# Performance work log

Hardware: AMD Instinct MI355X
Metric: run time of the kernel (lower is better)

Reference implementation:

```python
import jax, jax.numpy as jnp
import numpy as np

N1 = 8000   # solute nodes
N2 = 8000   # solvent nodes
E = 128000  # edges per graph side (avg degree 16)
B = 128     # number of graphs in the batch
NFEAT, NHID, NCLS = 128, 256, 512
D = 2 * NCLS   # Set2Set input dim (1024)
H = D          # LSTM hidden = input_dim in DGL Set2Set


def setup_inputs() -> dict:
    key = jax.random.key(0)
    ks = jax.random.split(key, 24)
    w = lambda k, shp, fan: (jax.random.normal(k, shp, jnp.float32) / np.sqrt(fan))
    inp = {}
    inp["x1"] = jax.random.normal(ks[0], (N1, NFEAT), jnp.float32)
    inp["x2"] = jax.random.normal(ks[1], (N2, NFEAT), jnp.float32)
    inp["src1"] = jax.random.randint(ks[2], (E,), 0, N1, jnp.int32)
    inp["dst1"] = jax.random.randint(ks[3], (E,), 0, N1, jnp.int32)
    inp["src2"] = jax.random.randint(ks[4], (E,), 0, N2, jnp.int32)
    inp["dst2"] = jax.random.randint(ks[5], (E,), 0, N2, jnp.int32)
    inp["gid1"] = jnp.sort(jax.random.randint(ks[6], (N1,), 0, B, jnp.int32))
    inp["gid2"] = jnp.sort(jax.random.randint(ks[7], (N2,), 0, B, jnp.int32))
    # GraphConv weights (DGL stores W as [in, out]) + biases
    inp["W_gc1"] = w(ks[8], (NFEAT, NHID), NFEAT); inp["b_gc1"] = jnp.zeros((NHID,), jnp.float32)
    inp["W_gc2"] = w(ks[9], (NHID, NCLS), NHID);   inp["b_gc2"] = jnp.zeros((NCLS,), jnp.float32)
    inp["W_gc3"] = w(ks[10], (NFEAT, NHID), NFEAT); inp["b_gc3"] = jnp.zeros((NHID,), jnp.float32)
    inp["W_gc4"] = w(ks[11], (NHID, NCLS), NHID);   inp["b_gc4"] = jnp.zeros((NCLS,), jnp.float32)
    # Set2Set LSTM (input = 2*D, hidden = H), torch gate order i,f,g,o
    inp["W_ih"] = w(ks[12], (4 * H, 2 * D), 2 * D)
    inp["W_hh"] = w(ks[13], (4 * H, H), H)
    inp["b_ih"] = jnp.zeros((4 * H,), jnp.float32)
    inp["b_hh"] = jnp.zeros((4 * H,), jnp.float32)
    # MLP head
    inp["W_fc1"] = w(ks[14], (1024, 4096), 4096); inp["b_fc1"] = jnp.zeros((1024,), jnp.float32)
    inp["W_fc2"] = w(ks[15], (512, 1024), 1024);  inp["b_fc2"] = jnp.zeros((512,), jnp.float32)
    inp["W_fc3"] = w(ks[16], (1, 512), 512);      inp["b_fc3"] = jnp.zeros((1,), jnp.float32)
    return inp


def _gconv(x, src, dst, W, b, n):
    # DGL GraphConv, norm='both': D_out^{-1/2} scaling at src, sum over in-edges, D_in^{-1/2} at dst
    ones = jnp.ones(src.shape[0], x.dtype)
    outd = jnp.clip(jax.ops.segment_sum(ones, src, num_segments=n), 1.0)
    ind = jnp.clip(jax.ops.segment_sum(ones, dst, num_segments=n), 1.0)
    h = (x * (outd ** -0.5)[:, None]) @ W
    agg = jax.ops.segment_sum(h[src], dst, num_segments=n)   # sparse neighbor aggregation
    return agg * (ind ** -0.5)[:, None] + b


def _set2set(x, gid, Wih, Whh, bih, bhh):
    # DGL Set2Set, n_iters=2, 1-layer LSTM; x: [N, D], gid: [N] graph membership
    d = x.shape[1]
    q_star = jnp.zeros((B, 2 * d), x.dtype)
    h = jnp.zeros((B, d), x.dtype)
    c = jnp.zeros((B, d), x.dtype)
    for _ in range(2):
        gates = q_star @ Wih.T + h @ Whh.T + bih + bhh
        i, f, g, o = jnp.split(gates, 4, axis=1)
        c = jax.nn.sigmoid(f) * c + jax.nn.sigmoid(i) * jnp.tanh(g)
        h = jax.nn.sigmoid(o) * jnp.tanh(c)
        e = jnp.sum(x * h[gid], axis=1)                       # per-node attention logit
        m = jax.ops.segment_max(e, gid, num_segments=B)
        ex = jnp.exp(e - m[gid])
        s = jax.ops.segment_sum(ex, gid, num_segments=B)
        alpha = ex / s[gid]                                   # segment softmax
        r = jax.ops.segment_sum(alpha[:, None] * x, gid, num_segments=B)
        q_star = jnp.concatenate([h, r], axis=1)
    return q_star


def reference(x1, x2, src1, dst1, src2, dst2, gid1, gid2,
              W_gc1, b_gc1, W_gc2, b_gc2, W_gc3, b_gc3, W_gc4, b_gc4,
              W_ih, W_hh, b_ih, b_hh,
              W_fc1, b_fc1, W_fc2, b_fc2, W_fc3, b_fc3):
    s = jax.nn.relu(_gconv(x1, src1, dst1, W_gc1, b_gc1, N1))
    s = _gconv(s, src1, dst1, W_gc2, b_gc2, N1)
    v = jax.nn.relu(_gconv(x2, src2, dst2, W_gc3, b_gc3, N2))
    v = _gconv(v, src2, dst2, W_gc4, b_gc4, N2)
    # len_map = len1.T @ len2 == same-graph indicator for binary membership matrices
    len_map = (gid1[:, None] == gid2[None, :]).astype(s.dtype)
    imap = jnp.tanh(s @ v.T) * len_map                        # [N1, N2]
    solvent_prime = imap.T @ s                                # [N2, NCLS]
    solute_prime = imap @ v                                   # [N1, NCLS]
    sf = jnp.concatenate([s, solute_prime], axis=1)           # [N1, 2*NCLS]
    vf = jnp.concatenate([v, solvent_prime], axis=1)
    ss = _set2set(sf, gid1, W_ih, W_hh, b_ih, b_hh)           # [B, 4*NCLS]
    vs = _set2set(vf, gid2, W_ih, W_hh, b_ih, b_hh)
    z = jnp.concatenate([ss, vs], axis=1)                     # [B, 4096]
    z = jax.nn.relu(z @ W_fc1.T + b_fc1)
    z = jax.nn.relu(z @ W_fc2.T + b_fc2)
    return z @ W_fc3.T + b_fc3                                # [B, 1]
```

## Files before the change

kernel.cpp:

```cpp
#include <hip/hip_runtime.h>

#define DEV __device__ __forceinline__

typedef _Float16 half8 __attribute__((ext_vector_type(8)));
typedef _Float16 half4_t __attribute__((ext_vector_type(4)));
typedef float f32x4 __attribute__((ext_vector_type(4)));

DEV float ftanh(float x){
  float ax = fabsf(x);
  float e = __expf(-2.f*ax);
  float t = (1.f - e)/(1.f + e);
  return x < 0.f ? -t : t;
}
DEV float fsigm(float x){ return 1.f/(1.f + expf(-x)); }
DEV float wredsum(float v){
  #pragma unroll
  for (int o=32;o;o>>=1) v += __shfl_xor(v,o,64);
  return v;
}
DEV f32x4 MF(half8 a, half8 b, f32x4 c){
  return __builtin_amdgcn_mfma_f32_16x16x32_f16(a,b,c,0,0,0);
}
DEV void split8(float4 a0, float4 a1, half8& h, half8& l){
  float f[8] = {a0.x,a0.y,a0.z,a0.w,a1.x,a1.y,a1.z,a1.w};
  #pragma unroll
  for (int e=0;e<8;++e){
    _Float16 hh = (_Float16)f[e];
    h[e] = hh;
    l[e] = (_Float16)(f[e] - (float)hh);
  }
}

__global__ void k_zero_i32(int* __restrict__ p, int n){
  int i = blockIdx.x*256 + threadIdx.x; if (i<n) p[i]=0;
}

__global__ void k_hist2(const int* __restrict__ s1, const int* __restrict__ d1, int E1,
                        int* __restrict__ co1, int* __restrict__ ci1,
                        const int* __restrict__ s2, const int* __restrict__ d2, int E2,
                        int* __restrict__ co2, int* __restrict__ ci2){
  int e = blockIdx.x*256 + threadIdx.x;
  if (e < E1){ atomicAdd(&co1[s1[e]],1); atomicAdd(&ci1[d1[e]],1); }
  int f = e - E1;
  if (f >= 0 && f < E2){ atomicAdd(&co2[s2[f]],1); atomicAdd(&ci2[d2[f]],1); }
}

__global__ void k_scan2(const int* __restrict__ c1, int n1, int* __restrict__ r1,
                        const int* __restrict__ c2, int n2, int* __restrict__ r2){
  __shared__ int sm[1024];
  const int* cnt = blockIdx.x ? c2 : c1;
  int*       row = blockIdx.x ? r2 : r1;
  int n          = blockIdx.x ? n2 : n1;
  int t = threadIdx.x;
  int per = n/1024 + 1;
  int st = t*per;
  int s = 0;
  for (int i=st;i<st+per;++i) if (i<n) s += cnt[i];
  sm[t]=s; __syncthreads();
  for (int o=1;o<1024;o<<=1){
    int v = (t>=o)? sm[t-o]:0;
    __syncthreads();
    sm[t] += v;
    __syncthreads();
  }
  int base = sm[t]-s;
  for (int i=st;i<st+per;++i){
    if (i<=n) row[i]=base;
    if (i<n) base += cnt[i];
  }
}

__global__ void k_scale2(const int* __restrict__ co1, const int* __restrict__ ci1, int n1,
                         float* __restrict__ os1, float* __restrict__ is1,
                         const int* __restrict__ co2, const int* __restrict__ ci2, int n2,
                         float* __restrict__ os2, float* __restrict__ is2){
  int i = blockIdx.x*256+threadIdx.x;
  if (i<n1){
    int a = co1[i] > 1 ? co1[i] : 1;
    int b = ci1[i] > 1 ? ci1[i] : 1;
    os1[i] = 1.f/sqrtf((float)a);
    is1[i] = 1.f/sqrtf((float)b);
  }
  int j = i - n1;
  if (j>=0 && j<n2){
    int a = co2[j] > 1 ? co2[j] : 1;
    int b = ci2[j] > 1 ? ci2[j] : 1;
    os2[j] = 1.f/sqrtf((float)a);
    is2[j] = 1.f/sqrtf((float)b);
  }
}

__global__ void k_scatter2(const int* __restrict__ s1, const int* __restrict__ d1, int E1,
                           const int* __restrict__ row1, int* __restrict__ cur1, int* __restrict__ csr1,
                           const int* __restrict__ s2, const int* __restrict__ d2, int E2,
                           const int* __restrict__ row2, int* __restrict__ cur2, int* __restrict__ csr2){
  int e = blockIdx.x*256+threadIdx.x;
  if (e<E1){ int d=d1[e]; int p=atomicAdd(&cur1[d],1); csr1[row1[d]+p]=s1[e]; }
  int f = e - E1;
  if (f>=0 && f<E2){ int d=d2[f]; int p=atomicAdd(&cur2[d],1); csr2[row2[d]+p]=s2[f]; }
}

__global__ void k_goff2(const int* __restrict__ g1, int n1, int* __restrict__ o1,
                        const int* __restrict__ g2, int n2, int* __restrict__ o2, int B,
                        int* __restrict__ pb1, int* __restrict__ gm1,
                        int* __restrict__ pb2, int* __restrict__ gm2){
  __shared__ int sc[2][256];
  int t = threadIdx.x;
  const int* gid = (t>=256)? g2 : g1;
  int*      goff = (t>=256)? o2 : o1;
  int n          = (t>=256)? n2 : n1;
  const int side = t>>8, q = t & 255;
  if (q<=B){
    int lo=0, hi=n;
    while (lo<hi){ int mid=(lo+hi)>>1; if (gid[mid]<q) lo=mid+1; else hi=mid; }
    goff[q]=lo;
  }
  __syncthreads();
  int pc = 0;
  if (q < B){
    const int* go = side ? o2 : o1;
    int c = go[q+1]-go[q]; if (c>128) c=128;
    pc = (c+31)&~31;
  }
  sc[side][q] = pc;
  __syncthreads();
  for (int o=1;o<B;o<<=1){
    int v = (q>=o && q<B) ? sc[side][q-o] : 0;
    __syncthreads();
    if (q<B) sc[side][q] += v;
    __syncthreads();
  }
  if (q < B){
    int incl = sc[side][q];
    int pbv  = incl - pc;
    int* pb = side ? pb2 : pb1;
    int* gm = side ? gm2 : gm1;
    pb[q] = pbv;
    if (q == B-1) pb[B] = incl;
    int nb = pc>>5, b0 = pbv>>5;
    for (int k=0;k<nb;++k) gm[b0+k] = q;
  }
}

__global__ void k_agg_h(const float* __restrict__ x, int ldx, const float* __restrict__ osc,
                        const int* __restrict__ row, const int* __restrict__ csr,
                        _Float16* __restrict__ oh, _Float16* __restrict__ ol, int n, int f4shift){
  int F4 = 1<<f4shift;
  int node = blockIdx.x*(256>>f4shift) + (threadIdx.x>>f4shift);
  if (node>=n) return;
  int fc = threadIdx.x & (F4-1);
  int F = F4<<2;
  int rs=row[node], re=row[node+1];
  float ax=0, ay=0, az=0, aw=0;
  if (osc){
    for (int e=rs;e<re;++e){
      int s = csr[e];
      float sc = osc[s];
      const float4 v = *(const float4*)(x + (size_t)s*ldx + (fc<<2));
      ax += sc*v.x; ay += sc*v.y; az += sc*v.z; aw += sc*v.w;
    }
  } else {
    int e = rs;
    for (; e+1<re; e+=2){
      int s0 = csr[e], s1 = csr[e+1];
      const float4 v0 = *(const float4*)(x + (size_t)s0*ldx + (fc<<2));
      const float4 v1 = *(const float4*)(x + (size_t)s1*ldx + (fc<<2));
      ax += v0.x+v1.x; ay += v0.y+v1.y; az += v0.z+v1.z; aw += v0.w+v1.w;
    }
    if (e<re){
      int s0 = csr[e];
      const float4 v0 = *(const float4*)(x + (size_t)s0*ldx + (fc<<2));
      ax += v0.x; ay += v0.y; az += v0.z; aw += v0.w;
    }
  }
  half4_t hv, lv;
  hv.x = (_Float16)ax; lv.x = (_Float16)(ax - (float)hv.x);
  hv.y = (_Float16)ay; lv.y = (_Float16)(ay - (float)hv.y);
  hv.z = (_Float16)az; lv.z = (_Float16)(az - (float)hv.z);
  hv.w = (_Float16)aw; lv.w = (_Float16)(aw - (float)hv.w);
  size_t o = (size_t)node*F + (fc<<2);
  *(half4_t*)(oh + o) = hv;
  *(half4_t*)(ol + o) = lv;
}

__global__ void k_wpack4(const float* __restrict__ W0, const float* __restrict__ W1,
                         const float* __restrict__ W2, const float* __restrict__ W3,
                         _Float16* __restrict__ h0, _Float16* __restrict__ l0,
                         _Float16* __restrict__ h1, _Float16* __restrict__ l1,
                         _Float16* __restrict__ h2, _Float16* __restrict__ l2,
                         _Float16* __restrict__ h3, _Float16* __restrict__ l3){
  int w = blockIdx.y;
  const float* W = (w==0)?W0:(w==1)?W1:(w==2)?W2:W3;
  _Float16* oh = (w==0)?h0:(w==1)?h1:(w==2)?h2:h3;
  _Float16* ol = (w==0)?l0:(w==1)?l1:(w==2)?l2:l3;
  int K   = (w&1)? 256 : 128;
  int nsh = (w&1)? 9 : 8;
  int i = blockIdx.x*256 + threadIdx.x;
  if (i >= (K<<nsh)) return;
  int k = i >> nsh, n = i & ((1<<nsh)-1);
  float v = W[i];
  _Float16 h = (_Float16)v;
  _Float16 l = (_Float16)(v - (float)h);
  size_t p = (((size_t)(k>>3)<<nsh) + n)*8 + (k&7);
  oh[p] = h; ol[p] = l;
}

__global__ __launch_bounds__(256)
void k_wpackT(const float* __restrict__ W, int ldw, int N,
              _Float16* __restrict__ Bh, _Float16* __restrict__ Bl){
  __shared__ float st[32][260];
  const int k0 = (int)blockIdx.x << 8;
  const int n0 = (int)blockIdx.y << 5;
  const int t = threadIdx.x;
  const int r = t >> 3, la = t & 7;
  const float* src = W + (size_t)(n0 + r)*ldw + k0;
  #pragma unroll
  for (int q=0;q<8;++q){
    int f = (la<<2) + (q<<5);
    *(float4*)&st[r][f] = *(const float4*)(src + f);
  }
  __syncthreads();
  const int nl = t & 31;
  #pragma unroll
  for (int j=0;j<4;++j){
    int kbl = (t>>5) + (j<<3);
    half8 h8, l8;
    #pragma unroll
    for (int e=0;e<8;++e){
      float v = st[nl][(kbl<<3)+e];
      _Float16 hh = (_Float16)v;
      h8[e]=hh; l8[e]=(_Float16)(v-(float)hh);
    }
    size_t a = ((size_t)((k0>>3)+kbl)*N + n0 + nl)*8;
    *(half8*)(Bh + a) = h8;
    *(half8*)(Bl + a) = l8;
  }
}

__global__ __launch_bounds__(256)
void k_gconv_mfma(const _Float16* __restrict__ Ah0, const _Float16* __restrict__ Al0,
                  const _Float16* __restrict__ Ah1, const _Float16* __restrict__ Al1,
                  const _Float16* __restrict__ Bh0, const _Float16* __restrict__ Bl0,
                  const _Float16* __restrict__ Bh1, const _Float16* __restrict__ Bl1,
                  float* __restrict__ C0, float* __restrict__ C1, int ldc,
                  int M0, int M1, int N, int K,
                  const float* __restrict__ rs0, const float* __restrict__ rs1,
                  const float* __restrict__ bi0, const float* __restrict__ bi1, int relu,
                  const float* __restrict__ po0, const float* __restrict__ po1)
{
  __shared__ __align__(16) _Float16 As[2][4096];
  __shared__ __align__(16) _Float16 Bs[2][4096];

  const int gx = gridDim.x, gxy = gridDim.x*gridDim.y;
  const int nwg = gxy*2;
  int fid = blockIdx.x + gx*blockIdx.y + gxy*blockIdx.z;
  int q = nwg>>3, r = nwg&7;
  int xcd = fid & 7, idx = fid >> 3;
  int sid = (xcd<r ? xcd*(q+1) : r*(q+1)+(xcd-r)*q) + idx;
  const int z  = sid / gxy;  int rem = sid - z*gxy;
  const int by = rem / gx,  bx = rem - by*gx;

  const _Float16* Ah = z ? Ah1 : Ah0;
  const _Float16* Al = z ? Al1 : Al0;
  const _Float16* Bh = z ? Bh1 : Bh0;
  const _Float16* Bl = z ? Bl1 : Bl0;
  float*       C  = z ? C1 : C0;
  const float* rsc = z ? rs1 : rs0;
  const float* bia = z ? bi1 : bi0;
  const float* po  = z ? po1 : po0;
  const int M = z ? M1 : M0;

  const int row0 = by << 7;
  const int col0 = bx << 7;
  if (row0 >= ((M+127)&~127)) return;

  const int tid = threadIdx.x;
  const int am  = tid >> 2;
  const int akb = tid & 3;
  const int bn  = tid & 127;
  const int bkb = tid >> 7;
  const int wid = tid >> 6, lane = tid & 63;
  const int wr = wid >> 1, wc = wid & 1;
  const int lr = lane & 15, lg = lane >> 4;

  const size_t ldb8 = (size_t)N * 8;
  f32x4 acc[4][4] = {};

  const int kpt = K >> 5;
  const int nt  = 3 * kpt;

  half8 ga0, ga1, gb0, gb1;
  {
    const _Float16* Ap = Ah + (size_t)(row0 + am) * K + (akb<<3);
    ga0 = *(const half8*)(Ap);
    ga1 = *(const half8*)(Ap + (size_t)64 * K);
    const _Float16* Bp = Bh + (size_t)bkb * ldb8 + (size_t)(col0 + bn) * 8;
    gb0 = *(const half8*)(Bp);
    gb1 = *(const half8*)(Bp + 2*ldb8);
  }
  *(half8*)&As[0][(akb*128 + am)*8]        = ga0;
  *(half8*)&As[0][(akb*128 + am + 64)*8]   = ga1;
  *(half8*)&Bs[0][(bkb*128 + bn)*8]        = gb0;
  *(half8*)&Bs[0][((bkb+2)*128 + bn)*8]    = gb1;
  __syncthreads();

  int term = 0, kk = 32;
  if (kk == K){ kk = 0; term = 1; }
  for (int t = 0; t < nt; ++t){
    const int cb = t & 1;
    if (t + 1 < nt){
      const _Float16* Asrc = (term == 1) ? Al : Ah;
      const _Float16* Bsrc = (term == 2) ? Bl : Bh;
      const _Float16* Ap = Asrc + (size_t)(row0 + am) * K + kk + (akb<<3);
      ga0 = *(const half8*)(Ap);
      ga1 = *(const half8*)(Ap + (size_t)64 * K);
      const _Float16* Bp = Bsrc + (size_t)((kk>>3) + bkb) * ldb8 + (size_t)(col0 + bn) * 8;
      gb0 = *(const half8*)(Bp);
      gb1 = *(const half8*)(Bp + 2*ldb8);
      kk += 32; if (kk == K){ kk = 0; ++term; }
    }
    {
      const _Float16* Abase = &As[cb][((lg<<7) + (wr<<6) + lr)<<3];
      const _Float16* Bbase = &Bs[cb][((lg<<7) + (wc<<6) + lr)<<3];
      half8 af[4], bf[4];
      #pragma unroll
      for (int i=0;i<4;++i){
        af[i] = *(const half8*)(Abase + i*128);
        bf[i] = *(const half8*)(Bbase + i*128);
      }
      #pragma unroll
      for (int mi=0; mi<4; ++mi){
        #pragma unroll
        for (int ni=0; ni<4; ++ni){
          acc[mi][ni] = __builtin_amdgcn_mfma_f32_16x16x32_f16(af[mi], bf[ni], acc[mi][ni], 0, 0, 0);
        }
      }
    }
    if (t + 1 < nt){
      const int nb_ = cb ^ 1;
      *(half8*)&As[nb_][(akb*128 + am)*8]      = ga0;
      *(half8*)&As[nb_][(akb*128 + am + 64)*8] = ga1;
      *(half8*)&Bs[nb_][(bkb*128 + bn)*8]      = gb0;
      *(half8*)&Bs[nb_][((bkb+2)*128 + bn)*8]  = gb1;
    }
    __syncthreads();
  }

  #pragma unroll
  for (int ni = 0; ni < 4; ++ni){
    int cc = col0 + (wc<<6) + (ni<<4) + lr;
    float bv = bia ? bia[cc] : 0.f;
    #pragma unroll
    for (int mi = 0; mi < 4; ++mi){
      int rbase = row0 + (wr<<6) + (mi<<4) + (lg<<2);
      #pragma unroll
      for (int j = 0; j < 4; ++j){
        int rr = rbase + j;
        if (rr < M){
          float rs_ = rsc ? rsc[rr] : 1.f;
          float v = acc[mi][ni][j]*rs_ + bv;
          if (relu) v = fmaxf(v, 0.f);
          if (po) v *= po[rr];
          C[(size_t)rr*ldc + cc] = v;
        }
      }
    }
  }
}

__global__ __launch_bounds__(256)
void k_pack(const float* __restrict__ sf, const float* __restrict__ vf,
            const int* __restrict__ go1, const int* __restrict__ go2,
            const int* __restrict__ pb1, const int* __restrict__ pb2,
            const int* __restrict__ gm1, const int* __restrict__ gm2,
            _Float16* __restrict__ p1h, _Float16* __restrict__ p1l,
            _Float16* __restrict__ p2h, _Float16* __restrict__ p2l, int B)
{
  __shared__ float st[32][516];
  const int side = blockIdx.y;
  const float* x = side ? vf : sf;
  const int* go = side ? go2 : go1;
  const int* pb = side ? pb2 : pb1;
  const int* gm = side ? gm2 : gm1;
  _Float16* ph = side ? p2h : p1h;
  _Float16* pl = side ? p2l : p1l;
  const int u = blockIdx.x;
  if (u*32 >= pb[B]) return;
  const int g = gm[u];
  const int j0 = u*32 - pb[g];
  const int base = go[g];
  int cnt = go[g+1]-base; if (cnt>128) cnt=128;
  const int t = threadIdx.x;
  const int r = t>>3, f0 = (t&7)<<2;
  const bool valid = (j0 + r) < cnt;
  const float* src = x + (size_t)(base + j0 + r)*1024;
  #pragma unroll
  for (int q=0;q<16;++q){
    int f = f0 + (q<<5);
    float4 vv;
    if (valid) vv = *(const float4*)(src + f);
    else { vv.x=0.f; vv.y=0.f; vv.z=0.f; vv.w=0.f; }
    *(float4*)&st[r][f] = vv;
  }
  __syncthreads();
  #pragma unroll
  for (int q=0;q<8;++q){
    int u2 = t + (q<<8);
    int jg = u2>>9, f = u2&511;
    half8 h8, l8;
    #pragma unroll
    for (int e=0;e<8;++e){
      float vvv = st[(jg<<3)+e][f];
      _Float16 hh = (_Float16)vvv;
      h8[e]=hh; l8[e]=(_Float16)(vvv-(float)hh);
    }
    size_t a = ((size_t)((u<<2)+jg)<<12) + ((size_t)f<<3);
    *(half8*)(ph + a) = h8;
    *(half8*)(pl + a) = l8;
  }
}

__global__ __launch_bounds__(256)
void k_T(const float* __restrict__ sf, const float* __restrict__ vf,
         const int* __restrict__ go1, const int* __restrict__ go2,
         _Float16* __restrict__ Th, _Float16* __restrict__ Tl, int B)
{
  __shared__ __align__(16) _Float16 Ahs[64*136 + 8];
  __shared__ __align__(16) _Float16 Als[64*136 + 8];
  __shared__ __align__(16) _Float16 Bhs[2][2048];
  __shared__ __align__(16) _Float16 Bls[2][2048];
  const int g = blockIdx.x, rt = blockIdx.y;
  int gR = go1[g]; int c1 = go1[g+1]-gR; if (c1>128) c1=128;
  int gO = go2[g]; int c2 = go2[g+1]-gO; if (c2>128) c2=128;
  const int c1_32 = (c1+31)&~31, c2_32 = (c2+31)&~31;
  if ((rt<<4) >= c1_32 || c2_32 == 0) return;
  const int tid = threadIdx.x;
  {
    const int r = tid >> 4;
    const int f0 = (tid & 15) << 5;
    const int row = (rt<<4) + r;
    const bool val = row < c1;
    const float* src = sf + (size_t)(gR + row)*1024 + f0;
    #pragma unroll
    for (int q=0;q<4;++q){
      float4 v0, v1;
      if (val){
        v0 = *(const float4*)(src + (q<<3));
        v1 = *(const float4*)(src + (q<<3) + 4);
      } else {
        v0.x=0.f; v0.y=0.f; v0.z=0.f; v0.w=0.f; v1 = v0;
      }
      half8 h,l; split8(v0,v1,h,l);
      const int a = ((f0>>3) + q)*136 + (r<<3);
      *(half8*)&Ahs[a] = h; *(half8*)&Als[a] = l;
    }
  }
  const int w = tid>>6, lane = tid&63, lr = lane&15, lg = lane>>4;
  const int bc = tid>>2, bfg = tid&3, bf = bfg<<3;
  const int bwr = (bfg<<9) + ((bc ^ (bfg<<2))<<3);
  const int ncc = (c2_32 + 63) >> 6;
  _Float16* T0h = Th + ((size_t)g<<14);
  _Float16* T0l = Tl + ((size_t)g<<14);
  _Float16* T1h = Th + ((size_t)(B + g)<<14);
  _Float16* T1l = Tl + ((size_t)(B + g)<<14);
  for (int cc=0; cc<ncc; ++cc){
    const int cbase = cc<<6;
    const int colr = cbase + bc;
    const bool bval = colr < c2;
    const float* bsrc = vf + (size_t)(gO + colr)*1024 + bf;
    {
      float4 v0, v1;
      if (bval){ v0 = *(const float4*)(bsrc); v1 = *(const float4*)(bsrc + 4); }
      else { v0.x=0.f; v0.y=0.f; v0.z=0.f; v0.w=0.f; v1 = v0; }
      half8 h,l; split8(v0,v1,h,l);
      *(half8*)&Bhs[0][bwr] = h; *(half8*)&Bls[0][bwr] = l;
    }
    __syncthreads();
    f32x4 acc = {0.f,0.f,0.f,0.f};
    const int col_l = (w<<4) + lr;
    const int ba = (lg<<9) + ((col_l ^ (lg<<2))<<3);
    for (int kc=0; kc<16; ++kc){
      float4 p0, p1;
      if (kc+1<16){
        if (bval){
          const float* s = bsrc + ((kc+1)<<5);
          p0 = *(const float4*)s; p1 = *(const float4*)(s + 4);
        } else { p0.x=0.f; p0.y=0.f; p0.z=0.f; p0.w=0.f; p1 = p0; }
      }
      const int aa = ((kc<<2)+lg)*136 + (lr<<3);
      half8 ah = *(const half8*)&Ahs[aa];
      half8 al = *(const half8*)&Als[aa];
      half8 bh = *(const half8*)&Bhs[kc&1][ba];
      half8 bl = *(const half8*)&Bls[kc&1][ba];
      acc = MF(ah,bh,acc);
      acc = MF(al,bh,acc);
      acc = MF(ah,bl,acc);
      if (kc+1<16){
        half8 h,l; split8(p0,p1,h,l);
        *(half8*)&Bhs[(kc+1)&1][bwr] = h; *(half8*)&Bls[(kc+1)&1][bwr] = l;
      }
      __syncthreads();
    }
    const int col = cbase + col_l;
    if (col < c2_32){
      half4_t t1h, t1l;
      #pragma unroll
      for (int qq=0;qq<4;++qq){
        int r = (rt<<4) + (lg<<2) + qq;
        float t = (r < c1 && col < c2) ? ftanh(acc[qq]) : 0.f;
        _Float16 hh = (_Float16)t;
        _Float16 ll = (_Float16)(t - (float)hh);
        T0h[(r<<7) + col] = hh;
        T0l[(r<<7) + col] = ll;
        t1h[qq] = hh; t1l[qq] = ll;
      }
      const int r0 = (rt<<4) + (lg<<2);
      *(half4_t*)&T1h[(col<<7) + r0] = t1h;
      *(half4_t*)&T1l[(col<<7) + r0] = t1l;
    }
  }
}

__global__ __launch_bounds__(256)
void k_apply(const _Float16* __restrict__ Th, const _Float16* __restrict__ Tl,
             const _Float16* __restrict__ p1h, const _Float16* __restrict__ p1l,
             const _Float16* __restrict__ p2h, const _Float16* __restrict__ p2l,
             const int* __restrict__ go1, const int* __restrict__ go2,
             const int* __restrict__ pb1, const int* __restrict__ pb2,
             float* __restrict__ sf, float* __restrict__ vf, int B)
{
  const int side = blockIdx.x, g = blockIdx.y, ft = blockIdx.z;
  const int* goR = side ? go2 : go1;
  const int* goO = side ? go1 : go2;
  const int* pbO = side ? pb1 : pb2;
  const _Float16* oph = side ? p1h : p2h;
  const _Float16* opl = side ? p1l : p2l;
  float* outp = side ? vf : sf;
  int gR = goR[g]; int cR = goR[g+1]-gR; if (cR>128) cR=128;
  int gO = goO[g]; int cO = goO[g+1]-gO; if (cO>128) cO=128;
  if (cR <= 0) return;
  const int pO = pbO[g];
  const int cO32 = (cO+31)&~31;
  const int MR = ((cR+15)&~15)>>4;
  const _Float16* Tph = Th + ((size_t)(side*B + g)<<14);
  const _Float16* Tpl = Tl + ((size_t)(side*B + g)<<14);
  const int tid = threadIdx.x, w = tid>>6, lane = tid&63;
  const int lr = lane&15, lg = lane>>4;
  const int f0 = (ft<<8) + (w<<6);
  for (int rc = 0; rc < MR; rc += 4){
    f32x4 acc[4][4];
    #pragma unroll
    for (int a_=0;a_<4;++a_)
      #pragma unroll
      for (int b_=0;b_<4;++b_) acc[a_][b_] = (f32x4){0.f,0.f,0.f,0.f};
    for (int k0=0; k0<cO32; k0+=32){
      half8 bh[4], bl[4];
      #pragma unroll
      for (int nj=0;nj<4;++nj){
        size_t a = ((size_t)((pO + k0)>>3) + lg)*4096 + (size_t)(f0 + (nj<<4) + lr)*8;
        bh[nj] = *(const half8*)(oph + a);
        bl[nj] = *(const half8*)(opl + a);
      }
      #pragma unroll
      for (int mi=0;mi<4;++mi){
        if (rc + mi < MR){
          int a = ((((rc+mi)<<4) + lr)<<7) + k0 + (lg<<3);
          half8 th_ = *(const half8*)&Tph[a];
          half8 tl_ = *(const half8*)&Tpl[a];
          #pragma unroll
          for (int nj=0;nj<4;++nj){
            acc[mi][nj] = MF(th_, bh[nj], acc[mi][nj]);
            acc[mi][nj] = MF(tl_, bh[nj], acc[mi][nj]);
            acc[mi][nj] = MF(th_, bl[nj], acc[mi][nj]);
          }
        }
      }
    }
    #pragma unroll
    for (int mi=0;mi<4;++mi){
      if (rc + mi < MR){
        #pragma unroll
        for (int nj=0;nj<4;++nj){
          #pragma unroll
          for (int qq=0;qq<4;++qq){
            int r = (((rc+mi)<<4)) + (lg<<2) + qq;
            if (r < cR)
              outp[(size_t)(gR + r)*1024 + 512 + f0 + (nj<<4) + lr] = acc[mi][nj][qq];
          }
        }
      }
    }
  }
}

__global__ __launch_bounds__(256)
void k_gemmsk(const float* __restrict__ Ab, size_t AsideOff, int lda,
              const float* __restrict__ Bm, int ldb,
              float* __restrict__ P, int M, int N, int kchunk)
{
  __shared__ float As[2][16][132];
  __shared__ float Bs[2][16][68];
  const int tid = threadIdx.x;
  const int col0 = (int)blockIdx.x << 6;
  const int kbeg = (int)blockIdx.z * kchunk;
  const float* A = Ab + (size_t)blockIdx.y * AsideOff;
  const int ar = tid >> 1, ak = (tid & 1) << 3;
  const int br = tid >> 2, bk = (tid & 3) << 2;
  const int tx = tid & 15, ty = tid >> 4;
  const float* Arow = A + (size_t)ar * lda + kbeg + ak;
  const float* Brow = Bm + (size_t)(col0 + br) * ldb + kbeg + bk;
  float acc[8][4] = {};
  float4 a0 = *(const float4*)(Arow);
  float4 a1 = *(const float4*)(Arow + 4);
  float4 b0 = *(const float4*)(Brow);
  As[0][ak+0][ar]=a0.x; As[0][ak+1][ar]=a0.y; As[0][ak+2][ar]=a0.z; As[0][ak+3][ar]=a0.w;
  As[0][ak+4][ar]=a1.x; As[0][ak+5][ar]=a1.y; As[0][ak+6][ar]=a1.z; As[0][ak+7][ar]=a1.w;
  Bs[0][bk+0][br]=b0.x; Bs[0][bk+1][br]=b0.y; Bs[0][bk+2][br]=b0.z; Bs[0][bk+3][br]=b0.w;
  __syncthreads();
  const int nt = kchunk >> 4;
  for (int t = 0; t < nt; ++t){
    const int cb = t & 1;
    if (t + 1 < nt){
      int k0 = (t + 1) << 4;
      a0 = *(const float4*)(Arow + k0);
      a1 = *(const float4*)(Arow + k0 + 4);
      b0 = *(const float4*)(Brow + k0);
    }
    #pragma unroll
    for (int kk = 0; kk < 16; ++kk){
      float4 b4 = *(const float4*)&Bs[cb][kk][tx << 2];
      float4 a4 = *(const float4*)&As[cb][kk][ty << 3];
      float4 a5 = *(const float4*)&As[cb][kk][(ty << 3) + 4];
      acc[0][0]+=a4.x*b4.x; acc[0][1]+=a4.x*b4.y; acc[0][2]+=a4.x*b4.z; acc[0][3]+=a4.x*b4.w;
      acc[1][0]+=a4.y*b4.x; acc[1][1]+=a4.y*b4.y; acc[1][2]+=a4.y*b4.z; acc[1][3]+=a4.y*b4.w;
      acc[2][0]+=a4.z*b4.x; acc[2][1]+=a4.z*b4.y; acc[2][2]+=a4.z*b4.z; acc[2][3]+=a4.z*b4.w;
      acc[3][0]+=a4.w*b4.x; acc[3][1]+=a4.w*b4.y; acc[3][2]+=a4.w*b4.z; acc[3][3]+=a4.w*b4.w;
      acc[4][0]+=a5.x*b4.x; acc[4][1]+=a5.x*b4.y; acc[4][2]+=a5.x*b4.z; acc[4][3]+=a5.x*b4.w;
      acc[5][0]+=a5.y*b4.x; acc[5][1]+=a5.y*b4.y; acc[5][2]+=a5.y*b4.z; acc[5][3]+=a5.y*b4.w;
      acc[6][0]+=a5.z*b4.x; acc[6][1]+=a5.z*b4.y; acc[6][2]+=a5.z*b4.z; acc[6][3]+=a5.z*b4.w;
      acc[7][0]+=a5.w*b4.x; acc[7][1]+=a5.w*b4.y; acc[7][2]+=a5.w*b4.z; acc[7][3]+=a5.w*b4.w;
    }
    if (t + 1 < nt){
      const int nb = cb ^ 1;
      As[nb][ak+0][ar]=a0.x; As[nb][ak+1][ar]=a0.y; As[nb][ak+2][ar]=a0.z; As[nb][ak+3][ar]=a0.w;
      As[nb][ak+4][ar]=a1.x; As[nb][ak+5][ar]=a1.y; As[nb][ak+6][ar]=a1.z; As[nb][ak+7][ar]=a1.w;
      Bs[nb][bk+0][br]=b0.x; Bs[nb][bk+1][br]=b0.y; Bs[nb][bk+2][br]=b0.z; Bs[nb][bk+3][br]=b0.w;
    }
    __syncthreads();
  }
  float* Pz = P + (size_t)(blockIdx.y*gridDim.z + blockIdx.z) * M * N;
  #pragma unroll
  for (int i = 0; i < 8; ++i){
    int rr = (ty << 3) + i;
    float4 v = {acc[i][0], acc[i][1], acc[i][2], acc[i][3]};
    *(float4*)(Pz + (size_t)rr*N + col0 + (tx<<2)) = v;
  }
}

__global__ __launch_bounds__(256)
void k_gemmsk_h(const float* __restrict__ Ab, size_t AsideOff, int lda,
                const _Float16* __restrict__ Bhp, const _Float16* __restrict__ Blp,
                float* __restrict__ P, int N, int kchunk)
{
  __shared__ __align__(16) _Float16 Ahs[2][4096];
  __shared__ __align__(16) _Float16 Als[2][4096];
  const int tid = threadIdx.x;
  const int col0 = (int)blockIdx.x << 7;
  const int kbeg = (int)blockIdx.z * kchunk;
  const float* A = Ab + (size_t)blockIdx.y * AsideOff;
  const int ar = tid >> 1, aq = (tid & 1) << 4;
  const int wid = tid>>6, lane = tid&63;
  const int wr = wid>>1, wc = wid&1;
  const int lr = lane&15, lg = lane>>4;
  const float* Arow = A + (size_t)ar*lda + kbeg + aq;
  const int akb = aq>>3;
  f32x4 acc[4][4] = {};
  const int nc = kchunk >> 5;
  float4 g0,g1,g2,g3;
  g0 = *(const float4*)(Arow);     g1 = *(const float4*)(Arow+4);
  g2 = *(const float4*)(Arow+8);   g3 = *(const float4*)(Arow+12);
  {
    half8 h,l;
    split8(g0,g1,h,l);
    *(half8*)&Ahs[0][(akb*128+ar)*8] = h;     *(half8*)&Als[0][(akb*128+ar)*8] = l;
    split8(g2,g3,h,l);
    *(half8*)&Ahs[0][((akb+1)*128+ar)*8] = h; *(half8*)&Als[0][((akb+1)*128+ar)*8] = l;
  }
  __syncthreads();
  for (int c=0;c<nc;++c){
    const int cb = c&1;
    if (c+1<nc){
      const float* p = Arow + ((c+1)<<5);
      g0 = *(const float4*)(p);    g1 = *(const float4*)(p+4);
      g2 = *(const float4*)(p+8);  g3 = *(const float4*)(p+12);
    }
    const size_t kb0 = (size_t)((kbeg + (c<<5)) >> 3) + lg;
    half8 bh[4], bl[4];
    #pragma unroll
    for (int ni=0;ni<4;++ni){
      size_t a = (kb0*N + col0 + (wc<<6) + (ni<<4) + lr)*8;
      bh[ni] = *(const half8*)(Bhp + a);
      bl[ni] = *(const half8*)(Blp + a);
    }
    #pragma unroll
    for (int mi=0;mi<4;++mi){
      int aa = ((lg<<7) + (wr<<6) + (mi<<4) + lr)<<3;
      half8 ah = *(const half8*)&Ahs[cb][aa];
      half8 al = *(const half8*)&Als[cb][aa];
      #pragma unroll
      for (int ni=0;ni<4;++ni){
        acc[mi][ni] = MF(ah,bh[ni],acc[mi][ni]);
        acc[mi][ni] = MF(al,bh[ni],acc[mi][ni]);
        acc[mi][ni] = MF(ah,bl[ni],acc[mi][ni]);
      }
    }
    if (c+1<nc){
      const int nb = cb^1;
      half8 h,l;
      split8(g0,g1,h,l);
      *(half8*)&Ahs[nb][(akb*128+ar)*8] = h;     *(half8*)&Als[nb][(akb*128+ar)*8] = l;
      split8(g2,g3,h,l);
      *(half8*)&Ahs[nb][((akb+1)*128+ar)*8] = h; *(half8*)&Als[nb][((akb+1)*128+ar)*8] = l;
    }
    __syncthreads();
  }
  float* Pz = P + (size_t)(blockIdx.y*gridDim.z + blockIdx.z)*128*N;
  #pragma unroll
  for (int mi=0;mi<4;++mi){
    #pragma unroll
    for (int ni=0;ni<4;++ni){
      int cc2 = col0 + (wc<<6) + (ni<<4) + lr;
      #pragma unroll
      for (int j=0;j<4;++j){
        int rr2 = (wr<<6) + (mi<<4) + (lg<<2) + j;
        Pz[(size_t)rr2*N + cc2] = acc[mi][ni][j];
      }
    }
  }
}

__global__ void k_red_bias(const float* __restrict__ P, int split, int MN, int N,
                           const float* __restrict__ bias, float* __restrict__ C, int relu){
  int i = blockIdx.x*256 + threadIdx.x;
  if (i >= MN) return;
  float v = bias[i & (N-1)];
  for (int s=0;s<split;++s) v += P[(size_t)s*MN + i];
  if (relu) v = fmaxf(v, 0.f);
  C[i] = v;
}

__global__ void k_lstm1(const float* __restrict__ bih, const float* __restrict__ bhh,
                        float* __restrict__ c1, float* __restrict__ h1){
  int j = blockIdx.x*256 + threadIdx.x;
  if (j >= 1024) return;
  float gi = bih[j]        + bhh[j];
  float gg = bih[j+2048]   + bhh[j+2048];
  float go = bih[j+3072]   + bhh[j+3072];
  float cc = fsigm(gi)*ftanh(gg);
  c1[j] = cc;
  h1[j] = fsigm(go)*ftanh(cc);
}

__global__ void k_gemv_u(const float* __restrict__ Wih, const float* __restrict__ Whh,
                         const float* __restrict__ bih, const float* __restrict__ bhh,
                         const float* __restrict__ h1, float* __restrict__ u){
  int w = (blockIdx.x*256 + threadIdx.x)>>6;
  int lane = threadIdx.x & 63;
  if (w >= 4096) return;
  const float* wi = Wih + (size_t)w*2048;
  const float* wh = Whh + (size_t)w*1024;
  float acc = 0.f;
  #pragma unroll
  for (int qq=0;qq<4;++qq){
    int o = qq*256 + (lane<<2);
    float4 hv = *(const float4*)(h1 + o);
    float4 a  = *(const float4*)(wi + o);
    float4 b  = *(const float4*)(wh + o);
    acc += hv.x*(a.x+b.x) + hv.y*(a.y+b.y) + hv.z*(a.z+b.z) + hv.w*(a.w+b.w);
  }
  acc = wredsum(acc);
  if (lane==0) u[w] = acc + bih[w] + bhh[w];
}

__global__ __launch_bounds__(256)
void k_attn(const float* __restrict__ sf, const float* __restrict__ vf,
            const int* __restrict__ go1, const int* __restrict__ go2,
            const float* __restrict__ hbase, size_t hSideOff, int hstride,
            float* __restrict__ outbase, size_t oSideOff, int ldout)
{
  __shared__ float hs[1024];
  __shared__ float ech[1024];
  __shared__ float red[8];
  int side = blockIdx.y;
  const float* x = side? vf : sf;
  const int* goff = side? go2 : go1;
  const float* hsrc = hbase + (size_t)side*hSideOff;
  float* outp = outbase + (size_t)side*oSideOff;
  int b = blockIdx.x, t = threadIdx.x;
  int i0 = goff[b], i1 = goff[b+1];
  int lane = t & 63, wv = t >> 6;
  { float4 hv = *(const float4*)(hsrc + (size_t)b*hstride + (t<<2));
    *(float4*)&hs[t<<2] = hv; }
  __syncthreads();
  float m = -3.0e38f, s = 0.f;
  float ax=0, ay=0, az=0, aw=0;
  for (int c = i0; c < i1; c += 1024){
    int ce = c + 1024; if (ce > i1) ce = i1;
    int n = ce - c;
    float wmax = -3.0e38f;
    for (int i = c + wv; i < ce; i += 4){
      const float* xr = x + (size_t)i*1024;
      float d = 0.f;
      #pragma unroll
      for (int qq=0;qq<4;++qq){
        int o = qq*256 + (lane<<2);
        float4 xv = *(const float4*)(xr+o);
        float4 h4 = *(const float4*)&hs[o];
        d += xv.x*h4.x + xv.y*h4.y + xv.z*h4.z + xv.w*h4.w;
      }
      d = wredsum(d);
      if (lane==0) ech[i-c] = d;
      wmax = fmaxf(wmax, d);
    }
    if (lane==0) red[wv] = wmax;
    __syncthreads();
    float cm = fmaxf(fmaxf(red[0],red[1]), fmaxf(red[2],red[3]));
    float nm = fmaxf(m, cm);
    float scale = __expf(m - nm);
    s *= scale; ax*=scale; ay*=scale; az*=scale; aw*=scale;
    float ps = 0.f;
    for (int k = t; k < n; k += 256) ps += __expf(ech[k]-nm);
    ps = wredsum(ps);
    __syncthreads();
    if (lane==0) red[wv] = ps;
    __syncthreads();
    s += red[0]+red[1]+red[2]+red[3];
    for (int k = 0; k < n; ++k){
      float w = __expf(ech[k]-nm);
      float4 xv = *(const float4*)(x + (size_t)(c+k)*1024 + (t<<2));
      ax += w*xv.x; ay += w*xv.y; az += w*xv.z; aw += w*xv.w;
    }
    m = nm;
    __syncthreads();
  }
  float inv = (i1>i0 && s>0.f) ? 1.f/s : 0.f;
  float4 o = {ax*inv, ay*inv, az*inv, aw*inv};
  *(float4*)(outp + (size_t)b*ldout + (t<<2)) = o;
}

__global__ void k_lstm2_red(const float* __restrict__ Pb, size_t PsideOff, int split,
                            const float* __restrict__ u, const float* __restrict__ c1,
                            float* __restrict__ z, int B){
  int idx = blockIdx.x*256 + threadIdx.x;
  if (idx >= B*1024) return;
  int side = blockIdx.y;
  const float* P = Pb + (size_t)side*PsideOff;
  int b = idx >> 10, j = idx & 1023;
  float gi=u[j], gf=u[j+1024], gg=u[j+2048], go=u[j+3072];
  const float* g = P + (size_t)b*4096;
  for (int s=0;s<split;++s){
    const float* gs = g + (size_t)s*B*4096;
    gi += gs[j]; gf += gs[j+1024]; gg += gs[j+2048]; go += gs[j+3072];
  }
  float cc = fsigm(gf)*c1[j] + fsigm(gi)*ftanh(gg);
  z[(size_t)b*4096 + side*2048 + j] = fsigm(go)*ftanh(cc);
}

__global__ void k_fc3(const float* __restrict__ z2, const float* __restrict__ w3,
                      const float* __restrict__ b3, float* __restrict__ out, int B){
  int wv = (blockIdx.x*256+threadIdx.x)>>6;
  int lane = threadIdx.x & 63;
  if (wv >= B) return;
  const float* zr = z2 + (size_t)wv*512;
  float acc=0.f;
  #pragma unroll
  for (int qq=0;qq<2;++qq){
    int o = qq*256 + (lane<<2);
    float4 a  = *(const float4*)(zr + o);
    float4 ww = *(const float4*)(w3 + o);
    acc += a.x*ww.x + a.y*ww.y + a.z*ww.z + a.w*ww.w;
  }
  acc = wredsum(acc);
  if (lane==0) out[wv] = acc + b3[0];
}

extern "C" void kernel_launch(void* const* d_in, const int* in_sizes, int n_in,
                              void* d_out, int out_size, void* d_ws, size_t ws_size,
                              hipStream_t stream)
{
  const float* x1  = (const float*)d_in[0];
  const float* x2  = (const float*)d_in[1];
  const int* src1  = (const int*)d_in[2];
  const int* dst1  = (const int*)d_in[3];
  const int* src2  = (const int*)d_in[4];
  const int* dst2  = (const int*)d_in[5];
  const int* gid1  = (const int*)d_in[6];
  const int* gid2  = (const int*)d_in[7];
  const float* Wg1 = (const float*)d_in[8];  const float* bg1 = (const float*)d_in[9];
  const float* Wg2 = (const float*)d_in[10]; const float* bg2 = (const float*)d_in[11];
  const float* Wg3 = (const float*)d_in[12]; const float* bg3 = (const float*)d_in[13];
  const float* Wg4 = (const float*)d_in[14]; const float* bg4 = (const float*)d_in[15];
  const float* Wih = (const float*)d_in[16]; const float* Whh = (const float*)d_in[17];
  const float* bih = (const float*)d_in[18]; const float* bhh = (const float*)d_in[19];
  const float* Wf1 = (const float*)d_in[20]; const float* bf1 = (const float*)d_in[21];
  const float* Wf2 = (const float*)d_in[22]; const float* bf2 = (const float*)d_in[23];
  const float* Wf3 = (const float*)d_in[24]; const float* bf3 = (const float*)d_in[25];
  float* out = (float*)d_out;

  const int N1 = in_sizes[0]/128;
  const int N2 = in_sizes[1]/128;
  const int E1 = in_sizes[2];
  const int E2 = in_sizes[4];
  const int B  = out_size;
  const int NM = N1>N2?N1:N2;

  char* base = (char*)d_ws; size_t off=0;
  auto alloc = [&](size_t bytes)->void*{ void* p = base+off; off += (bytes+255)&~(size_t)255; return p; };

  int* zr   = (int*)alloc(sizeof(int)*(size_t)(3*N1+3*N2));
  int* co1=zr, *ci1=zr+N1, *cur1=zr+2*N1;
  int* co2=zr+3*N1, *ci2=zr+3*N1+N2, *cur2=zr+3*N1+2*N2;
  int* row1 = (int*)alloc(sizeof(int)*(size_t)(N1+1));
  int* row2 = (int*)alloc(sizeof(int)*(size_t)(N2+1));
  int* csr1 = (int*)alloc(sizeof(int)*(size_t)E1);
  int* csr2 = (int*)alloc(sizeof(int)*(size_t)E2);
  int* go1  = (int*)alloc(sizeof(int)*(size_t)(B+1));
  int* go2  = (int*)alloc(sizeof(int)*(size_t)(B+1));
  int* pb1  = (int*)alloc(sizeof(int)*(size_t)(B+1));
  int* pb2  = (int*)alloc(sizeof(int)*(size_t)(B+1));
  int* gm1  = (int*)alloc(sizeof(int)*1024);
  int* gm2  = (int*)alloc(sizeof(int)*1024);
  float* os1 = (float*)alloc(sizeof(float)*(size_t)N1);
  float* is1 = (float*)alloc(sizeof(float)*(size_t)N1);
  float* os2 = (float*)alloc(sizeof(float)*(size_t)N2);
  float* is2 = (float*)alloc(sizeof(float)*(size_t)N2);
  _Float16* a1h = (_Float16*)alloc(sizeof(_Float16)*(size_t)(NM+128)*256);
  _Float16* a1l = (_Float16*)alloc(sizeof(_Float16)*(size_t)(NM+128)*256);
  _Float16* a2h = (_Float16*)alloc(sizeof(_Float16)*(size_t)(NM+128)*256);
  _Float16* a2l = (_Float16*)alloc(sizeof(_Float16)*(size_t)(NM+128)*256);
  _Float16* wg1h = (_Float16*)alloc(sizeof(_Float16)*32768);
  _Float16* wg1l = (_Float16*)alloc(sizeof(_Float16)*32768);
  _Float16* wg2h = (_Float16*)alloc(sizeof(_Float16)*131072);
  _Float16* wg2l = (_Float16*)alloc(sizeof(_Float16)*131072);
  _Float16* wg3h = (_Float16*)alloc(sizeof(_Float16)*32768);
  _Float16* wg3l = (_Float16*)alloc(sizeof(_Float16)*32768);
  _Float16* wg4h = (_Float16*)alloc(sizeof(_Float16)*131072);
  _Float16* wg4l = (_Float16*)alloc(sizeof(_Float16)*131072);
  _Float16* wihh = (_Float16*)alloc(sizeof(_Float16)*(size_t)4096*1024);
  _Float16* wihl = (_Float16*)alloc(sizeof(_Float16)*(size_t)4096*1024);
  _Float16* wf1h = (_Float16*)alloc(sizeof(_Float16)*(size_t)1024*4096);
  _Float16* wf1l = (_Float16*)alloc(sizeof(_Float16)*(size_t)1024*4096);
  float* sf  = (float*)alloc(sizeof(float)*(size_t)(N1+128)*1024);
  float* vf  = (float*)alloc(sizeof(float)*(size_t)(N2+128)*1024);
  float* h1 = (float*)alloc(sizeof(float)*1024);
  float* c1 = (float*)alloc(sizeof(float)*1024);
  float* u  = (float*)alloc(sizeof(float)*4096);
  float* r1 = (float*)alloc(sizeof(float)*(size_t)2*B*1024);
  float* z1 = (float*)alloc(sizeof(float)*(size_t)B*1024);
  float* z2 = (float*)alloc(sizeof(float)*(size_t)B*512);
  float* z  = (float*)alloc(sizeof(float)*(size_t)B*4096);
  _Float16* Tqh = (_Float16*)alloc(sizeof(_Float16)*(size_t)2*B*16384);
  _Float16* Tql = (_Float16*)alloc(sizeof(_Float16)*(size_t)2*B*16384);
  const int PN = ((NM + 32*B + 63)&~63) + 64;
  const size_t PE = (size_t)PN*512;
  size_t packedBytes = 4*PE*sizeof(_Float16);
  size_t pbufBytes   = sizeof(float)*(size_t)32*B*1024*4;
  char* uni = (char*)alloc(packedBytes > pbufBytes ? packedBytes : pbufBytes);
  _Float16* p1h = (_Float16*)uni;
  _Float16* p1l = p1h + PE;
  _Float16* p2h = p1l + PE;
  _Float16* p2l = p2h + PE;
  float* Pbuf = (float*)uni;
  if (off > ws_size) return;

  float* hb1 = sf + 512;
  float* hb2 = vf + 512;

  dim3 blk(256);

  k_wpack4<<<dim3(512,4),blk,0,stream>>>(Wg1,Wg2,Wg3,Wg4,
                                         wg1h,wg1l, wg2h,wg2l, wg3h,wg3l, wg4h,wg4l);
  k_wpackT<<<dim3(4,128),blk,0,stream>>>(Wih+1024, 2048, 4096, wihh, wihl);
  k_wpackT<<<dim3(16,32),blk,0,stream>>>(Wf1, 4096, 1024, wf1h, wf1l);

  k_zero_i32<<<(3*N1+3*N2+255)/256, blk, 0, stream>>>(zr, 3*N1+3*N2);
  k_hist2<<<(E1+E2+255)/256, blk, 0, stream>>>(src1,dst1,E1,co1,ci1, src2,dst2,E2,co2,ci2);
  k_scan2<<<2,1024,0,stream>>>(ci1,N1,row1, ci2,N2,row2);
  k_scale2<<<(N1+N2+255)/256,blk,0,stream>>>(co1,ci1,N1,os1,is1, co2,ci2,N2,os2,is2);
  k_scatter2<<<(E1+E2+255)/256,blk,0,stream>>>(src1,dst1,E1,row1,cur1,csr1, src2,dst2,E2,row2,cur2,csr2);
  k_goff2<<<1,512,0,stream>>>(gid1,N1,go1, gid2,N2,go2, B, pb1,gm1, pb2,gm2);

  int gy = (NM+127)/128;
  k_agg_h<<<(N1+7)/8,blk,0,stream>>>(x1,128, os1,row1,csr1, a1h,a1l, N1,5);
  k_agg_h<<<(N2+7)/8,blk,0,stream>>>(x2,128, os2,row2,csr2, a2h,a2l, N2,5);
  k_gconv_mfma<<<dim3(2,gy,2),blk,0,stream>>>(a1h,a1l, a2h,a2l,
                                              wg1h,wg1l, wg3h,wg3l,
                                              hb1,hb2,1024, N1,N2, 256,128,
                                              is1,is2, bg1,bg3, 1, os1,os2);
  k_agg_h<<<(N1+3)/4,blk,0,stream>>>(hb1,1024, nullptr,row1,csr1, a1h,a1l, N1,6);
  k_agg_h<<<(N2+3)/4,blk,0,stream>>>(hb2,1024, nullptr,row2,csr2, a2h,a2l, N2,6);
  k_gconv_mfma<<<dim3(4,gy,2),blk,0,stream>>>(a1h,a1l, a2h,a2l,
                                              wg2h,wg2l, wg4h,wg4l,
                                              sf,vf,1024, N1,N2, 512,256,
                                              is1,is2, bg2,bg4, 0, nullptr,nullptr);

  const int GMAX = NM/32 + B + 2;
  k_pack<<<dim3(GMAX,2),blk,0,stream>>>(sf,vf, go1,go2, pb1,pb2, gm1,gm2,
                                        p1h,p1l, p2h,p2l, B);
  k_T<<<dim3(B,8),blk,0,stream>>>(sf,vf, go1,go2, Tqh,Tql, B);
  k_apply<<<dim3(2,B,2),blk,0,stream>>>(Tqh,Tql, p1h,p1l, p2h,p2l,
                                        go1,go2, pb1,pb2, sf,vf, B);

  k_lstm1<<<4,blk,0,stream>>>(bih,bhh,c1,h1);
  k_gemv_u<<<1024,blk,0,stream>>>(Wih,Whh,bih,bhh,h1,u);

  k_attn<<<dim3(B,2),blk,0,stream>>>(sf,vf,go1,go2, h1,0,0, r1,(size_t)B*1024,1024);
  k_gemmsk_h<<<dim3(32,2,4),blk,0,stream>>>(r1,(size_t)B*1024,1024, wihh,wihl, Pbuf, 4096,256);
  k_lstm2_red<<<dim3((B*1024+255)/256,2),blk,0,stream>>>(Pbuf,(size_t)4*B*4096,4, u,c1, z,B);
  k_attn<<<dim3(B,2),blk,0,stream>>>(sf,vf,go1,go2, z,2048,4096, z+1024,2048,4096);

  k_gemmsk_h<<<dim3(8,1,32),blk,0,stream>>>(z,0,4096, wf1h,wf1l, Pbuf, 1024,128);
  k_red_bias<<<(B*1024+255)/256,blk,0,stream>>>(Pbuf,32,B*1024,1024,bf1,z1,1);
  k_gemmsk<<<dim3(8,1,8),blk,0,stream>>>(z1,0,1024, Wf2,1024, Pbuf, 128,512,128);
  k_red_bias<<<(B*512+255)/256,blk,0,stream>>>(Pbuf,8,B*512,512,bf2,z2,1);
  k_fc3<<<(B*64+255)/256,blk,0,stream>>>(z2,Wf3,bf3,out,B);
}
```

Before: 384.5 us.

## Fuse split-fp16 terms per k-step and read B fragments directly from global

The graph-conv GEMM previously ran three separate passes over K (hi*hi, lo*hi, hi*lo), each staging both A and B tiles through shared memory. It now stages the A hi and lo tiles together per k-chunk and issues all three MFMAs back to back, so the loop runs K/32 iterations instead of three times as many. The B fragments are loaded straight from global memory into registers, which cuts shared-memory traffic and the number of barriers. In exchange, B reads are uncoalesced and duplicated across waves, and register pressure rises.

New measurement: 381.4 us. About the same (-0.8%).

```diff
diff --git a/kernel.cpp b/kernel.cpp
--- a/kernel.cpp
+++ b/kernel.cpp
@@ -248,8 +248,8 @@
                   const float* __restrict__ bi0, const float* __restrict__ bi1, int relu,
                   const float* __restrict__ po0, const float* __restrict__ po1)
 {
-  __shared__ __align__(16) _Float16 As[2][4096];
-  __shared__ __align__(16) _Float16 Bs[2][4096];
+  __shared__ __align__(16) _Float16 Ahs[2][4096];
+  __shared__ __align__(16) _Float16 Als[2][4096];
 
   const int gx = gridDim.x, gxy = gridDim.x*gridDim.y;
   const int nwg = gxy*2;
@@ -277,71 +277,61 @@
   const int tid = threadIdx.x;
   const int am  = tid >> 2;
   const int akb = tid & 3;
-  const int bn  = tid & 127;
-  const int bkb = tid >> 7;
   const int wid = tid >> 6, lane = tid & 63;
   const int wr = wid >> 1, wc = wid & 1;
   const int lr = lane & 15, lg = lane >> 4;
 
-  const size_t ldb8 = (size_t)N * 8;
   f32x4 acc[4][4] = {};
-
-  const int kpt = K >> 5;
-  const int nt  = 3 * kpt;
-
-  half8 ga0, ga1, gb0, gb1;
-  {
-    const _Float16* Ap = Ah + (size_t)(row0 + am) * K + (akb<<3);
-    ga0 = *(const half8*)(Ap);
-    ga1 = *(const half8*)(Ap + (size_t)64 * K);
-    const _Float16* Bp = Bh + (size_t)bkb * ldb8 + (size_t)(col0 + bn) * 8;
-    gb0 = *(const half8*)(Bp);
-    gb1 = *(const half8*)(Bp + 2*ldb8);
-  }
-  *(half8*)&As[0][(akb*128 + am)*8]        = ga0;
-  *(half8*)&As[0][(akb*128 + am + 64)*8]   = ga1;
-  *(half8*)&Bs[0][(bkb*128 + bn)*8]        = gb0;
-  *(half8*)&Bs[0][((bkb+2)*128 + bn)*8]    = gb1;
+  const int nt = K >> 5;
+  const size_t rowK64 = (size_t)64 * K;
+  const _Float16* Aph = Ah + (size_t)(row0 + am) * K + (akb<<3);
+  const _Float16* Apl = Al + (size_t)(row0 + am) * K + (akb<<3);
+
+  half8 gh0 = *(const half8*)(Aph);
+  half8 gh1 = *(const half8*)(Aph + rowK64);
+  half8 gl0 = *(const half8*)(Apl);
+  half8 gl1 = *(const half8*)(Apl + rowK64);
+  *(half8*)&Ahs[0][(akb*128 + am)*8]      = gh0;
+  *(half8*)&Ahs[0][(akb*128 + am + 64)*8] = gh1;
+  *(half8*)&Als[0][(akb*128 + am)*8]      = gl0;
+  *(half8*)&Als[0][(akb*128 + am + 64)*8] = gl1;
   __syncthreads();
 
-  int term = 0, kk = 32;
-  if (kk == K){ kk = 0; term = 1; }
-  for (int t = 0; t < nt; ++t){
-    const int cb = t & 1;
-    if (t + 1 < nt){
-      const _Float16* Asrc = (term == 1) ? Al : Ah;
-      const _Float16* Bsrc = (term == 2) ? Bl : Bh;
-      const _Float16* Ap = Asrc + (size_t)(row0 + am) * K + kk + (akb<<3);
-      ga0 = *(const half8*)(Ap);
-      ga1 = *(const half8*)(Ap + (size_t)64 * K);
-      const _Float16* Bp = Bsrc + (size_t)((kk>>3) + bkb) * ldb8 + (size_t)(col0 + bn) * 8;
-      gb0 = *(const half8*)(Bp);
-      gb1 = *(const half8*)(Bp + 2*ldb8);
-      kk += 32; if (kk == K){ kk = 0; ++term; }
-    }
-    {
-      const _Float16* Abase = &As[cb][((lg<<7) + (wr<<6) + lr)<<3];
-      const _Float16* Bbase = &Bs[cb][((lg<<7) + (wc<<6) + lr)<<3];
-      half8 af[4], bf[4];
+  for (int c = 0; c < nt; ++c){
+    const int cb = c & 1;
+    if (c + 1 < nt){
+      const int k0 = (c + 1) << 5;
+      gh0 = *(const half8*)(Aph + k0);
+      gh1 = *(const half8*)(Aph + k0 + rowK64);
+      gl0 = *(const half8*)(Apl + k0);
+      gl1 = *(const half8*)(Apl + k0 + rowK64);
+    }
+    const size_t kb0 = (size_t)(c<<2) + lg;
+    half8 bh[4], bl[4];
+    #pragma unroll
+    for (int ni=0;ni<4;++ni){
+      size_t a = (kb0*N + col0 + (wc<<6) + (ni<<4) + lr)*8;
+      bh[ni] = *(const half8*)(Bh + a);
+      bl[ni] = *(const half8*)(Bl + a);
+    }
+    #pragma unroll
+    for (int mi=0;mi<4;++mi){
+      const int aa = ((lg<<7) + (wr<<6) + (mi<<4) + lr)<<3;
+      half8 ah = *(const half8*)&Ahs[cb][aa];
+      half8 al = *(const half8*)&Als[cb][aa];
       #pragma unroll
-      for (int i=0;i<4;++i){
-        af[i] = *(const half8*)(Abase + i*128);
-        bf[i] = *(const half8*)(Bbase + i*128);
-      }
-      #pragma unroll
-      for (int mi=0; mi<4; ++mi){
-        #pragma unroll
-        for (int ni=0; ni<4; ++ni){
-          acc[mi][ni] = __builtin_amdgcn_mfma_f32_16x16x32_f16(af[mi], bf[ni], acc[mi][ni], 0, 0, 0);
-        }
-      }
-    }
-    if (t + 1 < nt){
+      for (int ni=0;ni<4;++ni){
+        acc[mi][ni] = MF(ah, bh[ni], acc[mi][ni]);
+        acc[mi][ni] = MF(al, bh[ni], acc[mi][ni]);
+        acc[mi][ni] = MF(ah, bl[ni], acc[mi][ni]);
+      }
+    }
+    if (c + 1 < nt){
       const int nb_ = cb ^ 1;
-      *(half8*)&As[nb_][(akb*128 + am)*8]      = ga0;
-      *(half8*)&As[nb_][(akb*128 + am + 64)*8] = ga1;
-      *(half8*)&Bs[nb_][(bkb*128 + bn)*8]      = gb0;
-      *(half8*)&Bs[nb_][((bkb+2)*128 + bn)*8]  = gb1;
+      *(half8*)&Ahs[nb_][(akb*128 + am)*8]      = gh0;
+      *(half8*)&Ahs[nb_][(akb*128 + am + 64)*8] = gh1;
+      *(half8*)&Als[nb_][(akb*128 + am)*8]      = gl0;
+      *(half8*)&Als[nb_][(akb*128 + am + 64)*8] = gl1;
     }
     __syncthreads();
   }
```
